# Performance work log

Hardware: AMD Instinct MI355X
Metric: run time of the kernel (lower is better)

The kernel has to match this reference:

```python
import jax, jax.numpy as jnp
import numpy as np

HEADS = 8
DIM_HEAD = 40
SCALE = DIM_HEAD ** (-0.5)


def nearest_resize(m, H, W):
    # m: [B, 1, ih, iw] -> [B, H, W], torch F.interpolate mode='nearest' semantics
    _, _, ih, iw = m.shape
    hi = jnp.floor(jnp.arange(H) * (ih / H)).astype(jnp.int32)
    wi = jnp.floor(jnp.arange(W) * (iw / W)).astype(jnp.int32)
    return m[:, 0][:, hi][:, :, wi]


def split_heads(t):
    # [B, N, h*d] -> [(B*h), N, d]
    B, N, _ = t.shape
    return t.reshape(B, N, HEADS, DIM_HEAD).transpose(0, 2, 1, 3).reshape(B * HEADS, N, DIM_HEAD)


def setup_inputs() -> dict:
    key = jax.random.key(0)
    ks = jax.random.split(key, 9)
    d = 320
    inp = {
        'x': jax.random.normal(ks[0], (2, 3072, d), jnp.float32),
        'context': jax.random.normal(ks[1], (2, 3072, d), jnp.float32),
        'mask1': jax.random.uniform(ks[2], (2, 1, 512, 384), jnp.float32),
        'mask2': jax.random.uniform(ks[3], (2, 1, 512, 384), jnp.float32),
        'Wq': jax.random.normal(ks[4], (d, d), jnp.float32) * (d ** -0.5),
        'Wk': jax.random.normal(ks[5], (d, d), jnp.float32) * (d ** -0.5),
        'Wv': jax.random.normal(ks[6], (d, d), jnp.float32) * (d ** -0.5),
        'Wo': jax.random.normal(ks[7], (d, d), jnp.float32) * (d ** -0.5),
        'bo': jnp.zeros((d,), jnp.float32),
    }
    return inp


def reference(x, context, mask1, mask2, Wq, Wk, Wv, Wo, bo):
    b, n, _ = x.shape
    q = split_heads(x @ Wq)
    k = split_heads(context @ Wk)
    v = split_heads(context @ Wv)

    # fp32 attention scores (ATTN_PRECISION='fp32' path)
    sim = jnp.einsum('bid,bjd->bij', q.astype(jnp.float32), k.astype(jnp.float32)) * SCALE

    HW, hw = sim.shape[1], sim.shape[2]
    dx = int((HW // 12) ** 0.5)
    mH, mW = 4 * dx, 3 * dx
    dx2 = int((hw // 12) ** 0.5)
    mh, mw = 4 * dx2, 3 * dx2
    # mH=64 != 8 -> resize+mask branch
    m1 = nearest_resize(mask1, mH, mW) >= 0.5   # [b, mH, mW] bool
    m2 = nearest_resize(mask2, mh, mw) >= 0.5   # [b, mh, mw] bool
    attn_mask = m1.reshape(b, -1)[:, :, None] & m2.reshape(b, -1)[:, None, :]  # [b, HW, hw]
    attn_mask = jnp.repeat(attn_mask, HEADS, axis=0)  # [(b*h), HW, hw]

    neg = -jnp.finfo(sim.dtype).max
    sim = jnp.where(attn_mask, neg, sim)

    attn = jax.nn.softmax(sim, axis=-1).astype(v.dtype)
    out = jnp.einsum('bij,bjd->bid', attn, v)  # [(b*h), n, d]
    out = out.reshape(b, HEADS, n, DIM_HEAD).transpose(0, 2, 1, 3).reshape(b, n, HEADS * DIM_HEAD)
    return out @ Wo + bo
```

## Files before the change

kernel.cpp:

```cpp
#include <hip/hip_runtime.h>
#include <hip/hip_bf16.h>
#include <stdint.h>

typedef unsigned short u16;
typedef unsigned int u32;
typedef short bf16x8 __attribute__((ext_vector_type(8)));
typedef float f32x4 __attribute__((ext_vector_type(4)));
typedef float f32x16 __attribute__((ext_vector_type(16)));
typedef unsigned short u16x4 __attribute__((ext_vector_type(4)));
typedef int i32x4 __attribute__((ext_vector_type(4)));

#define NSEQ   3072
#define QSCALE 0.158113883008418966599446f

#define OFF_XB   ((size_t)0)
#define OFF_CB   ((size_t)3932160)
#define OFF_WT   ((size_t)7864320)
#define OFF_QG   ((size_t)8683520)
#define OFF_KG   ((size_t)12615680)
#define OFF_VT   ((size_t)16547840)
#define OFF_OB   ((size_t)21266432)
#define OFF_M1   ((size_t)25198592)
#define OFF_M2   ((size_t)25210880)

__device__ __forceinline__ u16 f2bf(float x) {
  __hip_bfloat16 h = __float2bfloat16(x);
  return __builtin_bit_cast(unsigned short, h);
}
__device__ __forceinline__ u32 pk(float lo, float hif) {
  return (u32)f2bf(lo) | ((u32)f2bf(hif) << 16);
}
__device__ __forceinline__ void lds_cp16(const void* g, void* l) {
  __builtin_amdgcn_global_load_lds((const __attribute__((address_space(1))) void*)g,
                                   (__attribute__((address_space(3))) void*)l, 16, 0, 0);
}

__global__ void prep_kernel(const float* __restrict__ x, const float* __restrict__ ctx,
                            const float* __restrict__ mask1, const float* __restrict__ mask2,
                            const float* __restrict__ Wq, const float* __restrict__ Wk,
                            const float* __restrict__ Wv, const float* __restrict__ Wo,
                            unsigned char* __restrict__ ws) {
  u16* xb = (u16*)(ws + OFF_XB);
  u16* cb = (u16*)(ws + OFF_CB);
  const int T0 = 491520;
  const int T1 = T0 + 491520;
  const int T2 = T1 + 102400;
  const int T3 = T2 + 1536;
  const int T4 = T3 + 1536;
  const int T5 = T4 + 49152;
  const int stride = gridDim.x * blockDim.x;
  for (int i = blockIdx.x * blockDim.x + threadIdx.x; i < T5; i += stride) {
    if (i < T1) {
      const float* src = (i < T0) ? x : ctx;
      u16* dst = (i < T0) ? xb : cb;
      int j = (i < T0) ? i : i - T0;
      float4 v = ((const float4*)src)[j];
      u16x4 o;
      o[0] = f2bf(v.x); o[1] = f2bf(v.y); o[2] = f2bf(v.z); o[3] = f2bf(v.w);
      *(u16x4*)(dst + (size_t)j * 4) = o;
    } else if (i < T2) {
      int j = i - T1;
      int m = j / 25600, rr = j % 25600;
      const float* W = (m == 0) ? Wq : (m == 1) ? Wk : (m == 2) ? Wv : Wo;
      u16* Wt = (u16*)(ws + OFF_WT + (size_t)m * 204800);
      int base = rr * 4, d = base / 320, k = base % 320;
      u16x4 o;
#pragma unroll
      for (int t = 0; t < 4; ++t) o[t] = f2bf(W[(size_t)(k + t) * 320 + d]);
      *(u16x4*)(Wt + (size_t)d * 320 + k) = o;
    } else if (i < T4) {
      bool isM1 = i < T3;
      int j = isM1 ? (i - T2) : (i - T3);
      const float* msk = isM1 ? mask1 : mask2;
      u16* dst = (u16*)(ws + (isM1 ? OFF_M1 : OFF_M2));
      int base = j * 4, b = base / 3072, r0 = base % 3072;
      u16x4 o;
#pragma unroll
      for (int t = 0; t < 4; ++t) {
        int rr = r0 + t, ih = rr / 48, iw = rr % 48;
        float mv = msk[(size_t)b * 196608 + ih * 3072 + iw * 8];
        bool on = mv >= 0.5f;
        o[t] = isM1 ? f2bf(on ? 1.0f : 0.0f) : f2bf(on ? -1e30f : 0.0f);
      }
      *(u16x4*)(dst + base) = o;
    } else {
      int j = i - T4;
      int idx8 = j * 8;
      int bh = idx8 / 24576, rem = idx8 % 24576;
      int pr = rem / 3072, c = rem % 3072;
      u16* Vt = (u16*)(ws + OFF_VT);
      u32 fill = (pr == 7) ? 0x3F803F80u : 0u;
      i32x4 z = {(int)fill, (int)fill, (int)fill, (int)fill};
      *(i32x4*)(Vt + (size_t)(bh * 48 + 40 + pr) * 3072 + c) = z;
    }
  }
}

__global__ __launch_bounds__(256) void gemm_all(unsigned char* __restrict__ ws,
                                                const float* __restrict__ bo,
                                                float* __restrict__ outf, int phase) {
  const u16* xb = (const u16*)(ws + OFF_XB);
  const u16* cb = (const u16*)(ws + OFF_CB);
  const int mode = phase ? 3 : (int)blockIdx.y;
  const u16* Ap; const u16* Bp;
  int bx = blockIdx.x;
  int mt, nt;
  if (mode == 0)      { Ap = xb; Bp = (const u16*)(ws + OFF_WT);            mt = bx / 5; nt = bx % 5; }
  else if (mode == 1) { Ap = cb; Bp = (const u16*)(ws + OFF_WT + 204800);   mt = bx / 5; nt = bx % 5; }
  else if (mode == 2) { Ap = (const u16*)(ws + OFF_WT + 2 * 204800); Bp = cb; mt = bx % 5; nt = bx / 5; }
  else                { Ap = (const u16*)(ws + OFF_OB); Bp = (const u16*)(ws + OFF_WT + 3 * 204800); mt = bx / 5; nt = bx % 5; }
  const int m0 = mt * 64, n0 = nt * 64;

  __shared__ u16 Als[64 * 32];
  __shared__ u16 Bls[64 * 32];

  const int tid = threadIdx.x;
  const int lane = tid & 63, w = tid >> 6;
  const int li = lane & 15, g = lane >> 4;

  f32x4 acc[4] = {};

  const int srow = tid >> 2, sslot = tid & 3;
  const int sgch = (sslot - ((srow >> 1) & 3)) & 3;
  const u16* aSrc = Ap + (size_t)(m0 + srow) * 320 + sgch * 8;
  const u16* bSrc = Bp + (size_t)(n0 + srow) * 320 + sgch * 8;

  const int arow = w * 16 + li;
  const int aoff = arow * 32 + (((g + ((arow >> 1) & 3)) & 3) * 8);

  for (int kt = 0; kt < 10; ++kt) {
    __syncthreads();
    lds_cp16(aSrc + kt * 32, (char*)Als + tid * 16);
    lds_cp16(bSrc + kt * 32, (char*)Bls + tid * 16);
    __syncthreads();
    bf16x8 af = *(const bf16x8*)(Als + aoff);
#pragma unroll
    for (int ct = 0; ct < 4; ++ct) {
      int brow = ct * 16 + li;
      bf16x8 bv = *(const bf16x8*)(Bls + brow * 32 + (((g + ((brow >> 1) & 3)) & 3) * 8));
      acc[ct] = __builtin_amdgcn_mfma_f32_16x16x32_bf16(af, bv, acc[ct], 0, 0, 0);
    }
  }

  const int erow = w * 16 + g * 4;
  if (mode == 0 || mode == 1) {
    u16* Og = (u16*)(ws + (mode == 0 ? OFF_QG : OFF_KG));
#pragma unroll
    for (int ct = 0; ct < 4; ++ct)
#pragma unroll
      for (int r = 0; r < 4; ++r) {
        float v = acc[ct][r];
        if (mode == 0) v *= QSCALE;
        Og[(size_t)(m0 + erow + r) * 320 + n0 + ct * 16 + li] = f2bf(v);
      }
  } else if (mode == 2) {
    u16* Vt = (u16*)(ws + OFF_VT);
#pragma unroll
    for (int ct = 0; ct < 4; ++ct)
#pragma unroll
      for (int r = 0; r < 4; ++r) {
        int d = m0 + erow + r;
        int h = d / 40, dd = d % 40;
        int n = n0 + ct * 16 + li;
        int b = (n >= 3072) ? 1 : 0;
        int nin = n - b * 3072;
        int bh = b * 8 + h;
        Vt[(size_t)(bh * 48 + dd) * 3072 + nin] = f2bf(acc[ct][r]);
      }
  } else {
#pragma unroll
    for (int ct = 0; ct < 4; ++ct) {
      float bias = bo[n0 + ct * 16 + li];
#pragma unroll
      for (int r = 0; r < 4; ++r)
        outf[(size_t)(m0 + erow + r) * 320 + n0 + ct * 16 + li] = acc[ct][r] + bias;
    }
  }
}

__global__ __launch_bounds__(256) void attn_kernel(unsigned char* __restrict__ ws) {
  const u16* Qg  = (const u16*)(ws + OFF_QG);
  const u16* Kg  = (const u16*)(ws + OFF_KG);
  const u16* Vt  = (const u16*)(ws + OFF_VT);
  const u16* m1i = (const u16*)(ws + OFF_M1);
  const u16* m2n = (const u16*)(ws + OFF_M2);
  u16* Ob = (u16*)(ws + OFF_OB);

  __shared__ u16 S[28928];

  const int tid = threadIdx.x;
  const int w = tid >> 6;
  const int lane = tid & 63;
  const int l31 = lane & 31, hi = lane >> 5;
  const int qw = w & 1, kw = w >> 1;

  const int p = blockIdx.x;
  const int logical = (p & 7) * 96 + (p >> 3);
  const int bh = logical / 48, qs = logical % 48;
  const int b = bh >> 3, h = bh & 7;
  const int q0 = qs * 64 + qw * 32;

  const u16* qrow = Qg + (size_t)(b * NSEQ + q0 + l31) * 320 + h * 40;
  bf16x8 qf0 = *(const bf16x8*)(qrow + hi * 8);
  bf16x8 qf1 = *(const bf16x8*)(qrow + 16 + hi * 8);
  bf16x8 qf2;
  {
    i32x4 real = *(const i32x4*)(qrow + 32);
    u16 m1v = m1i[b * NSEQ + q0 + l31];
    i32x4 mskv = {(int)(u32)m1v, 0, 0, 0};
    i32x4 sel = hi ? mskv : real;
    qf2 = __builtin_bit_cast(bf16x8, sel);
  }

  const u16* src[7]; int dst[7], sst[7], bst[7];
#pragma unroll
  for (int r = 0; r < 7; ++r) {
    int cid = r * 256 + tid;
    int s = (cid >= 896) ? 1 : 0;
    int c2 = cid - s * 896;
    if (c2 < 384) {
      int row = c2 >> 3, slot = c2 & 7, kc = slot ^ (row & 7);
      src[r] = Vt + (size_t)(bh * 48 + row) * 3072 + s * 1536 + kc * 8;
      sst[r] = 64; dst[r] = s * 6144 + c2 * 8; bst[r] = 3072;
    } else {
      int kcid = c2 - 384, row = kcid >> 3, slot = kcid & 7, kc = slot ^ (row & 7);
      src[r] = Kg + (size_t)(b * NSEQ + s * 1536 + row) * 320 + h * 40 + kc * 8;
      sst[r] = 64 * 320; dst[r] = 12288 + s * 8192 + kcid * 8; bst[r] = 4096;
    }
  }
  const u16* srcm = m2n + b * NSEQ + (tid >> 3) * 1536 + (tid & 7) * 8;
  const int dstm = 28672 + tid * 8;

  f32x16 oacc0 = {}, oacc1 = {};

  auto STAGE = [&](int bp) {
#pragma unroll
    for (int r = 0; r < 7; ++r) {
      lds_cp16(src[r], &S[dst[r] + bp * bst[r]]);
      src[r] += sst[r];
    }
    if (tid < 16) { lds_cp16(srcm, &S[dstm + bp * 128]); srcm += 64; }
  };

  auto COMPUTE = [&](int rb) {
    const u16* Kt = &S[12288 + (kw * 2 + rb) * 4096];
    const u16* Vl = &S[(kw * 2 + rb) * 3072];
    const u16* Ms = &S[28672 + rb * 128 + kw * 64];
    u16 m2v0 = Ms[l31], m2v1 = Ms[32 + l31];
    const int x = l31 & 7;
    const int rA0 = l31 * 64, rA1 = (l31 + 32) * 64;
    bf16x8 ka00 = *(const bf16x8*)(Kt + rA0 + ((hi ^ x) * 8));
    bf16x8 ka01 = *(const bf16x8*)(Kt + rA0 + (((2 + hi) ^ x) * 8));
    bf16x8 ka02 = *(const bf16x8*)(Kt + rA0 + (((4 + hi) ^ x) * 8));
    bf16x8 ka10 = *(const bf16x8*)(Kt + rA1 + ((hi ^ x) * 8));
    bf16x8 ka11 = *(const bf16x8*)(Kt + rA1 + (((2 + hi) ^ x) * 8));
    bf16x8 ka12 = *(const bf16x8*)(Kt + rA1 + (((4 + hi) ^ x) * 8));
    bf16x8 vf00 = *(const bf16x8*)(Vl + rA0 + ((hi ^ x) * 8));
    bf16x8 vf01 = *(const bf16x8*)(Vl + rA0 + (((2 + hi) ^ x) * 8));
    bf16x8 vf02 = *(const bf16x8*)(Vl + rA0 + (((4 + hi) ^ x) * 8));
    bf16x8 vf03 = *(const bf16x8*)(Vl + rA0 + (((6 + hi) ^ x) * 8));
    bf16x8 vf10 = *(const bf16x8*)(Vl + rA1 + ((hi ^ x) * 8));
    bf16x8 vf11 = *(const bf16x8*)(Vl + rA1 + (((2 + hi) ^ x) * 8));
    bf16x8 vf12 = *(const bf16x8*)(Vl + rA1 + (((4 + hi) ^ x) * 8));
    bf16x8 vf13 = *(const bf16x8*)(Vl + rA1 + (((6 + hi) ^ x) * 8));

    {
      i32x4 mv0 = {(int)(u32)m2v0, 0, 0, 0};
      i32x4 mv1 = {(int)(u32)m2v1, 0, 0, 0};
      ka02 = hi ? __builtin_bit_cast(bf16x8, mv0) : ka02;
      ka12 = hi ? __builtin_bit_cast(bf16x8, mv1) : ka12;
    }

    f32x16 s0 = {}, s1 = {};
    s0 = __builtin_amdgcn_mfma_f32_32x32x16_bf16(ka00, qf0, s0, 0, 0, 0);
    s0 = __builtin_amdgcn_mfma_f32_32x32x16_bf16(ka01, qf1, s0, 0, 0, 0);
    s0 = __builtin_amdgcn_mfma_f32_32x32x16_bf16(ka02, qf2, s0, 0, 0, 0);
    s1 = __builtin_amdgcn_mfma_f32_32x32x16_bf16(ka10, qf0, s1, 0, 0, 0);
    s1 = __builtin_amdgcn_mfma_f32_32x32x16_bf16(ka11, qf1, s1, 0, 0, 0);
    s1 = __builtin_amdgcn_mfma_f32_32x32x16_bf16(ka12, qf2, s1, 0, 0, 0);

    u32 w0[4][2], w1[4][2];
#pragma unroll
    for (int t = 0; t < 4; ++t) {
      w0[t][0] = pk(__expf(s0[4 * t]),     __expf(s0[4 * t + 1]));
      w0[t][1] = pk(__expf(s0[4 * t + 2]), __expf(s0[4 * t + 3]));
      w1[t][0] = pk(__expf(s1[4 * t]),     __expf(s1[4 * t + 1]));
      w1[t][1] = pk(__expf(s1[4 * t + 2]), __expf(s1[4 * t + 3]));
    }
    u32 r0[2][2], r1[2][2];
#pragma unroll
    for (int pp = 0; pp < 2; ++pp)
#pragma unroll
      for (int i = 0; i < 2; ++i) {
        u32 s0w = hi ? w0[2 * pp][i] : w0[2 * pp + 1][i];
        r0[pp][i] = (u32)__shfl_xor((int)s0w, 32);
        u32 s1w = hi ? w1[2 * pp][i] : w1[2 * pp + 1][i];
        r1[pp][i] = (u32)__shfl_xor((int)s1w, 32);
      }
#pragma unroll
    for (int ks = 0; ks < 4; ++ks) {
      const int pp = ks & 1;
      u32 a0, a1, a2, a3;
      if (ks < 2) {
        a0 = hi ? r0[pp][0] : w0[2 * pp][0];
        a1 = hi ? r0[pp][1] : w0[2 * pp][1];
        a2 = hi ? w0[2 * pp + 1][0] : r0[pp][0];
        a3 = hi ? w0[2 * pp + 1][1] : r0[pp][1];
      } else {
        a0 = hi ? r1[pp][0] : w1[2 * pp][0];
        a1 = hi ? r1[pp][1] : w1[2 * pp][1];
        a2 = hi ? w1[2 * pp + 1][0] : r1[pp][0];
        a3 = hi ? w1[2 * pp + 1][1] : r1[pp][1];
      }
      i32x4 av = {(int)a0, (int)a1, (int)a2, (int)a3};
      bf16x8 pa = __builtin_bit_cast(bf16x8, av);
      bf16x8 vA = (ks == 0) ? vf00 : (ks == 1) ? vf01 : (ks == 2) ? vf02 : vf03;
      bf16x8 vB = (ks == 0) ? vf10 : (ks == 1) ? vf11 : (ks == 2) ? vf12 : vf13;
      oacc0 = __builtin_amdgcn_mfma_f32_32x32x16_bf16(pa, vA, oacc0, 0, 0, 0);
      oacc1 = __builtin_amdgcn_mfma_f32_32x32x16_bf16(pa, vB, oacc1, 0, 0, 0);
    }
  };

  STAGE(0);
  __syncthreads();
  for (int t = 0; t < 24; t += 2) {
    STAGE(1);
    COMPUTE(0);
    __syncthreads();
    if (t + 2 < 24) STAGE(0);
    COMPUTE(1);
    __syncthreads();
  }

  float* PF = (float*)S;
  if (kw == 1) {
#pragma unroll
    for (int r = 0; r < 16; ++r) {
      PF[qw * 2048 + r * 64 + lane] = oacc0[r];
      PF[qw * 2048 + 1024 + r * 64 + lane] = oacc1[r];
    }
  }
  __syncthreads();
  if (kw == 0) {
#pragma unroll
    for (int r = 0; r < 16; ++r) {
      oacc0[r] += PF[qw * 2048 + r * 64 + lane];
      oacc1[r] += PF[qw * 2048 + 1024 + r * 64 + lane];
    }
#pragma unroll
    for (int r = 0; r < 16; ++r) {
      float L = __shfl(oacc1[r], hi * 32 + 15);
      float linv = 1.0f / L;
      const int row = q0 + (r & 3) + 8 * (r >> 2) + 4 * hi;
      u16* orow = Ob + (size_t)(b * NSEQ + row) * 320 + h * 40;
      orow[l31] = f2bf(oacc0[r] * linv);
      if (l31 < 8) orow[32 + l31] = f2bf(oacc1[r] * linv);
    }
  }
}

extern "C" void kernel_launch(void* const* d_in, const int* in_sizes, int n_in,
                              void* d_out, int out_size, void* d_ws, size_t ws_size,
                              hipStream_t stream) {
  const float* x     = (const float*)d_in[0];
  const float* ctx   = (const float*)d_in[1];
  const float* mask1 = (const float*)d_in[2];
  const float* mask2 = (const float*)d_in[3];
  const float* Wq    = (const float*)d_in[4];
  const float* Wk    = (const float*)d_in[5];
  const float* Wv    = (const float*)d_in[6];
  const float* Wo    = (const float*)d_in[7];
  const float* bo    = (const float*)d_in[8];
  unsigned char* ws  = (unsigned char*)d_ws;
  float* outp        = (float*)d_out;

  prep_kernel<<<2048, 256, 0, stream>>>(x, ctx, mask1, mask2, Wq, Wk, Wv, Wo, ws);
  gemm_all<<<dim3(480, 3), 256, 0, stream>>>(ws, nullptr, nullptr, 0);
  attn_kernel<<<768, 256, 0, stream>>>(ws);
  gemm_all<<<dim3(480, 1), 256, 0, stream>>>(ws, bo, outp, 1);
}
```

Measured before the change: 167.8 us.

## Fuse fp32-to-bf16 conversion into QKV GEMM and tile weight transpose

New measurement: 181.8 us. 8.3% more time.

```diff
diff --git a/kernel.cpp b/kernel.cpp
--- a/kernel.cpp
+++ b/kernel.cpp
@@ -11,10 +11,8 @@
 typedef int i32x4 __attribute__((ext_vector_type(4)));
 
 #define NSEQ   3072
-#define QSCALE 0.158113883008418966599446f
-
-#define OFF_XB   ((size_t)0)
-#define OFF_CB   ((size_t)3932160)
+#define QSCALE 0.2281101197f
+
 #define OFF_WT   ((size_t)7864320)
 #define OFF_QG   ((size_t)8683520)
 #define OFF_KG   ((size_t)12615680)
@@ -35,80 +33,67 @@
                                    (__attribute__((address_space(3))) void*)l, 16, 0, 0);
 }
 
-__global__ void prep_kernel(const float* __restrict__ x, const float* __restrict__ ctx,
-                            const float* __restrict__ mask1, const float* __restrict__ mask2,
+__global__ __launch_bounds__(256) void prep_kernel(const float* __restrict__ mask1,
+                            const float* __restrict__ mask2,
                             const float* __restrict__ Wq, const float* __restrict__ Wk,
                             const float* __restrict__ Wv, const float* __restrict__ Wo,
                             unsigned char* __restrict__ ws) {
-  u16* xb = (u16*)(ws + OFF_XB);
-  u16* cb = (u16*)(ws + OFF_CB);
-  const int T0 = 491520;
-  const int T1 = T0 + 491520;
-  const int T2 = T1 + 102400;
-  const int T3 = T2 + 1536;
-  const int T4 = T3 + 1536;
-  const int T5 = T4 + 49152;
-  const int stride = gridDim.x * blockDim.x;
-  for (int i = blockIdx.x * blockDim.x + threadIdx.x; i < T5; i += stride) {
-    if (i < T1) {
-      const float* src = (i < T0) ? x : ctx;
-      u16* dst = (i < T0) ? xb : cb;
-      int j = (i < T0) ? i : i - T0;
-      float4 v = ((const float4*)src)[j];
-      u16x4 o;
-      o[0] = f2bf(v.x); o[1] = f2bf(v.y); o[2] = f2bf(v.z); o[3] = f2bf(v.w);
-      *(u16x4*)(dst + (size_t)j * 4) = o;
-    } else if (i < T2) {
-      int j = i - T1;
-      int m = j / 25600, rr = j % 25600;
-      const float* W = (m == 0) ? Wq : (m == 1) ? Wk : (m == 2) ? Wv : Wo;
-      u16* Wt = (u16*)(ws + OFF_WT + (size_t)m * 204800);
-      int base = rr * 4, d = base / 320, k = base % 320;
-      u16x4 o;
-#pragma unroll
-      for (int t = 0; t < 4; ++t) o[t] = f2bf(W[(size_t)(k + t) * 320 + d]);
-      *(u16x4*)(Wt + (size_t)d * 320 + k) = o;
-    } else if (i < T4) {
-      bool isM1 = i < T3;
-      int j = isM1 ? (i - T2) : (i - T3);
-      const float* msk = isM1 ? mask1 : mask2;
-      u16* dst = (u16*)(ws + (isM1 ? OFF_M1 : OFF_M2));
-      int base = j * 4, b = base / 3072, r0 = base % 3072;
-      u16x4 o;
-#pragma unroll
-      for (int t = 0; t < 4; ++t) {
-        int rr = r0 + t, ih = rr / 48, iw = rr % 48;
-        float mv = msk[(size_t)b * 196608 + ih * 3072 + iw * 8];
-        bool on = mv >= 0.5f;
-        o[t] = isM1 ? f2bf(on ? 1.0f : 0.0f) : f2bf(on ? -1e30f : 0.0f);
-      }
-      *(u16x4*)(dst + base) = o;
-    } else {
-      int j = i - T4;
-      int idx8 = j * 8;
-      int bh = idx8 / 24576, rem = idx8 % 24576;
-      int pr = rem / 3072, c = rem % 3072;
-      u16* Vt = (u16*)(ws + OFF_VT);
-      u32 fill = (pr == 7) ? 0x3F803F80u : 0u;
-      i32x4 z = {(int)fill, (int)fill, (int)fill, (int)fill};
-      *(i32x4*)(Vt + (size_t)(bh * 48 + 40 + pr) * 3072 + c) = z;
-    }
-  }
-}
-
-__global__ __launch_bounds__(256) void gemm_all(unsigned char* __restrict__ ws,
-                                                const float* __restrict__ bo,
-                                                float* __restrict__ outf, int phase) {
-  const u16* xb = (const u16*)(ws + OFF_XB);
-  const u16* cb = (const u16*)(ws + OFF_CB);
-  const int mode = phase ? 3 : (int)blockIdx.y;
-  const u16* Ap; const u16* Bp;
-  int bx = blockIdx.x;
-  int mt, nt;
-  if (mode == 0)      { Ap = xb; Bp = (const u16*)(ws + OFF_WT);            mt = bx / 5; nt = bx % 5; }
-  else if (mode == 1) { Ap = cb; Bp = (const u16*)(ws + OFF_WT + 204800);   mt = bx / 5; nt = bx % 5; }
-  else if (mode == 2) { Ap = (const u16*)(ws + OFF_WT + 2 * 204800); Bp = cb; mt = bx % 5; nt = bx / 5; }
-  else                { Ap = (const u16*)(ws + OFF_OB); Bp = (const u16*)(ws + OFF_WT + 3 * 204800); mt = bx / 5; nt = bx % 5; }
+  const int blk = blockIdx.x, tid = threadIdx.x;
+  if (blk < 100) {
+    __shared__ float Lf[64][65];
+    const int wm = blk / 25, t25 = blk % 25, ti = t25 / 5, tj = t25 % 5;
+    const float* W = (wm == 0) ? Wq : (wm == 1) ? Wk : (wm == 2) ? Wv : Wo;
+    u16* Wt = (u16*)(ws + OFF_WT + (size_t)wm * 204800);
+#pragma unroll
+    for (int s = 0; s < 4; ++s) {
+      int row = (tid >> 4) + s * 16, c4 = (tid & 15) * 4;
+      float4 v = *(const float4*)&W[(size_t)(ti * 64 + row) * 320 + tj * 64 + c4];
+      Lf[row][c4] = v.x; Lf[row][c4 + 1] = v.y; Lf[row][c4 + 2] = v.z; Lf[row][c4 + 3] = v.w;
+    }
+    __syncthreads();
+    const int n = tid >> 2, kq = (tid & 3) * 16;
+    u16* dst = Wt + (size_t)(tj * 64 + n) * 320 + ti * 64 + kq;
+    i32x4 ov;
+#pragma unroll
+    for (int e = 0; e < 4; ++e) ov[e] = (int)pk(Lf[kq + 2 * e][n], Lf[kq + 2 * e + 1][n]);
+    *(i32x4*)(dst) = ov;
+#pragma unroll
+    for (int e = 0; e < 4; ++e) ov[e] = (int)pk(Lf[kq + 8 + 2 * e][n], Lf[kq + 9 + 2 * e][n]);
+    *(i32x4*)(dst + 8) = ov;
+  } else if (blk < 112) {
+    int j = (blk - 100) * 256 + tid;
+    bool isM1 = j < 1536;
+    int jj = isM1 ? j : j - 1536;
+    const float* msk = isM1 ? mask1 : mask2;
+    u16* dst = (u16*)(ws + (isM1 ? OFF_M1 : OFF_M2));
+    int base = jj * 4, b = base / 3072, r0 = base % 3072;
+    u16x4 o;
+#pragma unroll
+    for (int t = 0; t < 4; ++t) {
+      int rr = r0 + t, ih = rr / 48, iw = rr % 48;
+      float mv = msk[(size_t)b * 196608 + ih * 3072 + iw * 8];
+      bool on = mv >= 0.5f;
+      o[t] = isM1 ? f2bf(on ? 1.0f : 0.0f) : f2bf(on ? -1e30f : 0.0f);
+    }
+    *(u16x4*)(dst + base) = o;
+  } else {
+    int j = (blk - 112) * 256 + tid;
+    int idx8 = j * 8;
+    int bh = idx8 / 24576, rem = idx8 % 24576;
+    int pr = rem / 3072, c = rem % 3072;
+    u16* Vt = (u16*)(ws + OFF_VT);
+    u32 fill = (pr == 7) ? 0x3F803F80u : 0u;
+    i32x4 z = {(int)fill, (int)fill, (int)fill, (int)fill};
+    *(i32x4*)(Vt + (size_t)(bh * 48 + 40 + pr) * 3072 + c) = z;
+  }
+}
+
+__global__ __launch_bounds__(256) void gemm_qkv(const float* __restrict__ x,
+                                                const float* __restrict__ ctx,
+                                                unsigned char* __restrict__ ws) {
+  const int mode = (int)blockIdx.y;
+  int bx = blockIdx.x, mt, nt;
+  if (mode == 2) { mt = bx % 5; nt = bx / 5; } else { mt = bx / 5; nt = bx % 5; }
   const int m0 = mt * 64, n0 = nt * 64;
 
   __shared__ u16 Als[64 * 32];
@@ -117,21 +102,39 @@
   const int tid = threadIdx.x;
   const int lane = tid & 63, w = tid >> 6;
   const int li = lane & 15, g = lane >> 4;
-
   f32x4 acc[4] = {};
 
   const int srow = tid >> 2, sslot = tid & 3;
   const int sgch = (sslot - ((srow >> 1) & 3)) & 3;
-  const u16* aSrc = Ap + (size_t)(m0 + srow) * 320 + sgch * 8;
-  const u16* bSrc = Bp + (size_t)(n0 + srow) * 320 + sgch * 8;
+  const u16* Wbase = (const u16*)(ws + OFF_WT + (size_t)mode * 204800);
+  u16* Gls = (mode == 2) ? Als : Bls;
+  u16* Fls = (mode == 2) ? Bls : Als;
+  const int gbase = (mode == 2) ? m0 : n0;
+  const int fbase = (mode == 2) ? n0 : m0;
+  const float* F = (mode == 0) ? x : ctx;
+  const u16* gsrc = Wbase + (size_t)(gbase + srow) * 320 + sgch * 8;
+
+  const int frow = tid >> 2, fq = tid & 3;
+  const int fslot = (fq + ((frow >> 1) & 3)) & 3;
+  const float* fs0 = F + (size_t)(fbase + frow) * 320 + fq * 8;
+  u16* fdst = Fls + frow * 32 + fslot * 8;
 
   const int arow = w * 16 + li;
   const int aoff = arow * 32 + (((g + ((arow >> 1) & 3)) & 3) * 8);
 
+  float4 fa = *(const float4*)(fs0);
+  float4 fb = *(const float4*)(fs0 + 4);
   for (int kt = 0; kt < 10; ++kt) {
     __syncthreads();
-    lds_cp16(aSrc + kt * 32, (char*)Als + tid * 16);
-    lds_cp16(bSrc + kt * 32, (char*)Bls + tid * 16);
+    lds_cp16(gsrc + kt * 32, (char*)Gls + tid * 16);
+    i32x4 ov;
+    ov[0] = (int)pk(fa.x, fa.y); ov[1] = (int)pk(fa.z, fa.w);
+    ov[2] = (int)pk(fb.x, fb.y); ov[3] = (int)pk(fb.z, fb.w);
+    *(i32x4*)fdst = ov;
+    if (kt < 9) {
+      fa = *(const float4*)(fs0 + (kt + 1) * 32);
+      fb = *(const float4*)(fs0 + (kt + 1) * 32 + 4);
+    }
     __syncthreads();
     bf16x8 af = *(const bf16x8*)(Als + aoff);
 #pragma unroll
@@ -153,7 +156,7 @@
         if (mode == 0) v *= QSCALE;
         Og[(size_t)(m0 + erow + r) * 320 + n0 + ct * 16 + li] = f2bf(v);
       }
-  } else if (mode == 2) {
+  } else {
     u16* Vt = (u16*)(ws + OFF_VT);
 #pragma unroll
     for (int ct = 0; ct < 4; ++ct)
@@ -167,14 +170,54 @@
         int bh = b * 8 + h;
         Vt[(size_t)(bh * 48 + dd) * 3072 + nin] = f2bf(acc[ct][r]);
       }
-  } else {
+  }
+}
+
+__global__ __launch_bounds__(256) void gemm_out(unsigned char* __restrict__ ws,
+                                                const float* __restrict__ bo,
+                                                float* __restrict__ outf) {
+  const u16* Ap = (const u16*)(ws + OFF_OB);
+  const u16* Bp = (const u16*)(ws + OFF_WT + 3 * 204800);
+  int bx = blockIdx.x;
+  const int m0 = (bx / 5) * 64, n0 = (bx % 5) * 64;
+
+  __shared__ u16 Als[64 * 32];
+  __shared__ u16 Bls[64 * 32];
+
+  const int tid = threadIdx.x;
+  const int lane = tid & 63, w = tid >> 6;
+  const int li = lane & 15, g = lane >> 4;
+  f32x4 acc[4] = {};
+
+  const int srow = tid >> 2, sslot = tid & 3;
+  const int sgch = (sslot - ((srow >> 1) & 3)) & 3;
+  const u16* aSrc = Ap + (size_t)(m0 + srow) * 320 + sgch * 8;
+  const u16* bSrc = Bp + (size_t)(n0 + srow) * 320 + sgch * 8;
+
+  const int arow = w * 16 + li;
+  const int aoff = arow * 32 + (((g + ((arow >> 1) & 3)) & 3) * 8);
+
+  for (int kt = 0; kt < 10; ++kt) {
+    __syncthreads();
+    lds_cp16(aSrc + kt * 32, (char*)Als + tid * 16);
+    lds_cp16(bSrc + kt * 32, (char*)Bls + tid * 16);
+    __syncthreads();
+    bf16x8 af = *(const bf16x8*)(Als + aoff);
 #pragma unroll
     for (int ct = 0; ct < 4; ++ct) {
-      float bias = bo[n0 + ct * 16 + li];
-#pragma unroll
-      for (int r = 0; r < 4; ++r)
-        outf[(size_t)(m0 + erow + r) * 320 + n0 + ct * 16 + li] = acc[ct][r] + bias;
-    }
+      int brow = ct * 16 + li;
+      bf16x8 bv = *(const bf16x8*)(Bls + brow * 32 + (((g + ((brow >> 1) & 3)) & 3) * 8));
+      acc[ct] = __builtin_amdgcn_mfma_f32_16x16x32_bf16(af, bv, acc[ct], 0, 0, 0);
+    }
+  }
+
+  const int erow = w * 16 + g * 4;
+#pragma unroll
+  for (int ct = 0; ct < 4; ++ct) {
+    float bias = bo[n0 + ct * 16 + li];
+#pragma unroll
+    for (int r = 0; r < 4; ++r)
+      outf[(size_t)(m0 + erow + r) * 320 + n0 + ct * 16 + li] = acc[ct][r] + bias;
   }
 }
 
@@ -282,10 +325,10 @@
     u32 w0[4][2], w1[4][2];
 #pragma unroll
     for (int t = 0; t < 4; ++t) {
-      w0[t][0] = pk(__expf(s0[4 * t]),     __expf(s0[4 * t + 1]));
-      w0[t][1] = pk(__expf(s0[4 * t + 2]), __expf(s0[4 * t + 3]));
-      w1[t][0] = pk(__expf(s1[4 * t]),     __expf(s1[4 * t + 1]));
-      w1[t][1] = pk(__expf(s1[4 * t + 2]), __expf(s1[4 * t + 3]));
+      w0[t][0] = pk(exp2f(s0[4 * t]),     exp2f(s0[4 * t + 1]));
+      w0[t][1] = pk(exp2f(s0[4 * t + 2]), exp2f(s0[4 * t + 3]));
+      w1[t][0] = pk(exp2f(s1[4 * t]),     exp2f(s1[4 * t + 1]));
+      w1[t][1] = pk(exp2f(s1[4 * t + 2]), exp2f(s1[4 * t + 3]));
     }
     u32 r0[2][2], r1[2][2];
 #pragma unroll
@@ -374,8 +417,8 @@
   unsigned char* ws  = (unsigned char*)d_ws;
   float* outp        = (float*)d_out;
 
-  prep_kernel<<<2048, 256, 0, stream>>>(x, ctx, mask1, mask2, Wq, Wk, Wv, Wo, ws);
-  gemm_all<<<dim3(480, 3), 256, 0, stream>>>(ws, nullptr, nullptr, 0);
+  prep_kernel<<<304, 256, 0, stream>>>(mask1, mask2, Wq, Wk, Wv, Wo, ws);
+  gemm_qkv<<<dim3(480, 3), 256, 0, stream>>>(x, ctx, ws);
   attn_kernel<<<768, 256, 0, stream>>>(ws);
-  gemm_all<<<dim3(480, 1), 256, 0, stream>>>(ws, bo, outp, 1);
-}
+  gemm_out<<<480, 256, 0, stream>>>(ws, bo, outp);
+}
```
